# Performance work log

Measured on AMD Instinct MI355X. Metric: run time of the kernel, lower is better.

The kernel has to match this reference:

```python
import jax, jax.numpy as jnp
import numpy as np

B, C, D, J = 8, 2048, 128, 128

def setup_inputs() -> dict:
    key = jax.random.key(0)
    ks = jax.random.split(key, 24)
    s = 0.02
    inp = {
        "operation_features": jax.random.normal(ks[0], (B, C, D), jnp.float32),
        "relations": jax.random.randint(ks[1], (B, C - 2, 2), 0, C, jnp.int64),
        "begins_idx": jax.random.randint(ks[2], (B, J), 0, C, jnp.int64),
        "ends_idx": jax.random.randint(ks[3], (B, J), 0, C, jnp.int64),
        "same_type_mask": (jax.random.uniform(ks[4], (B, C, C)) > 0.5).astype(jnp.float32),
        # BeginEndEncoder
        "W_begin": jax.random.normal(ks[5], (D, D), jnp.float32) * s,
        "b_begin": jnp.zeros((D,), jnp.float32),
        "W_end": jax.random.normal(ks[6], (D, D), jnp.float32) * s,
        "b_end": jnp.zeros((D,), jnp.float32),
        # OperationTimeRelationEncoder.mix: Linear(3D -> D)
        "W_mix3": jax.random.normal(ks[7], (3 * D, D), jnp.float32) * s,
        "b_mix3": jnp.zeros((D,), jnp.float32),
        # SelfAttention (hidden_dim = D)
        "W_qkv": jax.random.normal(ks[8], (D, 3 * D), jnp.float32) * s,
        "b_qkv": jnp.zeros((3 * D,), jnp.float32),
        "w_score": jax.random.normal(ks[9], (2 * D,), jnp.float32) * s,
        "b_score": jnp.zeros((), jnp.float32),
        "W_out": jax.random.normal(ks[10], (D, D), jnp.float32) * s,
        "b_out": jnp.zeros((D,), jnp.float32),
        # block mix: Linear(2D -> D)
        "W_mix2": jax.random.normal(ks[11], (2 * D, D), jnp.float32) * s,
        "b_mix2": jnp.zeros((D,), jnp.float32),
    }
    return inp

def _gather_ops(ops, idx):
    # ops: [B,C,D], idx: [B,M] -> [B,M,D]  (torch.gather along dim 1 with expanded index)
    Bb, _, Dd = ops.shape
    M = idx.shape[1]
    return jnp.take_along_axis(ops, jnp.broadcast_to(idx[:, :, None], (Bb, M, Dd)), axis=1)

def reference(operation_features, relations, begins_idx, ends_idx, same_type_mask,
              W_begin, b_begin, W_end, b_end, W_mix3, b_mix3,
              W_qkv, b_qkv, w_score, b_score, W_out, b_out, W_mix2, b_mix2):
    ops = operation_features
    Dd = ops.shape[-1]
    # --- OperationTimeRelationEncoder ---
    pred = _gather_ops(ops, relations[..., 0])      # [B,C-2,D]
    succ = _gather_ops(ops, relations[..., 1])      # [B,C-2,D]
    concated = jnp.concatenate([ops[:, :-2, :], pred, succ], axis=-1)  # [B,C-2,3D]
    mixed = concated @ W_mix3 + b_mix3              # [B,C-2,D]
    begin_f = _gather_ops(ops, begins_idx) @ W_begin + b_begin  # [B,J,D]
    end_f = _gather_ops(ops, ends_idx) @ W_end + b_end
    begin = jnp.mean(begin_f, axis=1)               # [B,D]
    end = jnp.mean(end_f, axis=1)
    seq = jnp.concatenate([mixed, begin[:, None, :], end[:, None, :]], axis=1)  # [B,C,D]
    # --- SelfAttention (GAT-style additive score, decomposed to avoid CxCx2h blowup) ---
    qkv = ops @ W_qkv + b_qkv                       # [B,C,3D]
    q, k, v = jnp.split(qkv, 3, axis=-1)
    sq = q @ w_score[:Dd]                           # [B,C]  q_i . w_q
    sk = k @ w_score[Dd:]                           # [B,C]  k_j . w_k
    scores = jax.nn.leaky_relu(sq[:, :, None] + sk[:, None, :] + b_score)  # [B,C,C]
    attn = jax.nn.softmax(scores * same_type_mask, axis=-1)                # multiplicative mask, as in torch
    weighted = jnp.einsum('bij,bjd->bid', attn, v)  # [B,C,D]
    same_type = weighted @ W_out + b_out            # [B,C,D]
    # --- final mix ---
    return jnp.concatenate([seq, same_type], axis=-1) @ W_mix2 + b_mix2  # [B,C,D]
```

## Files before the change

### kernel.cpp

```cpp
#include <hip/hip_runtime.h>
#include <cstddef>

typedef __bf16 bf16;
typedef __bf16 bf16x4 __attribute__((ext_vector_type(4)));
typedef __bf16 bf16x8 __attribute__((ext_vector_type(8)));
typedef float  f32x4  __attribute__((ext_vector_type(4)));

#define MFMA16(a, b, c) __builtin_amdgcn_mfma_f32_16x16x32_bf16((a), (b), (c), 0, 0, 0)

#define BB 8
#define CC 2048
#define DD 128
#define JJN 128

#define WS_PK    ((size_t)0)
#define WS_OATT  ((size_t)4194304)
#define WS_OPS16 ((size_t)8388608)
#define WS_SQF   ((size_t)12582912)
#define WS_SKF   ((size_t)12648448)
#define WS_G1T   ((size_t)12713984)
#define WS_G2T   ((size_t)12746752)
#define WS_G3T   ((size_t)12779520)
#define WS_WCT   ((size_t)12812288)
#define WS_GBT   ((size_t)12845056)
#define WS_GET   ((size_t)12877824)
#define WS_UQK   ((size_t)12910592)
#define WS_BBM   ((size_t)12911104)
#define WS_BBB   ((size_t)12911616)
#define WS_BBE   ((size_t)12912128)
#define WS_SC    ((size_t)12912640)

__global__ __launch_bounds__(256) void k_prepcast(
    const float* __restrict__ ops, bf16* __restrict__ ops16,
    const float* __restrict__ Wmix3, const float* __restrict__ Wmix2,
    const float* __restrict__ Wout,  const float* __restrict__ Wbegin,
    const float* __restrict__ Wend,  const float* __restrict__ Wqkv,
    const float* __restrict__ bqkv,  const float* __restrict__ wscore,
    const float* __restrict__ bscore,const float* __restrict__ bmix3,
    const float* __restrict__ bout,  const float* __restrict__ bmix2,
    const float* __restrict__ bbegin,const float* __restrict__ bend,
    bf16* __restrict__ G1T, bf16* __restrict__ G2T, bf16* __restrict__ G3T,
    bf16* __restrict__ WCT, bf16* __restrict__ GBT, bf16* __restrict__ GET,
    bf16* __restrict__ uqk, float* __restrict__ BBM, float* __restrict__ BBB,
    float* __restrict__ BBE, float* __restrict__ sc)
{
    __shared__ bf16  LshT[128 * 132];
    __shared__ float Rsh[128 * 8];
    int wg = blockIdx.x;
    int t  = threadIdx.x;

    if (wg < 1024) {
        size_t i = (size_t)wg * 256 + t;
        f32x4 a = *(const f32x4*)(ops + i * 8);
        f32x4 b = *(const f32x4*)(ops + i * 8 + 4);
        bf16x8 o;
        #pragma unroll
        for (int e = 0; e < 4; ++e) { o[e] = (bf16)a[e]; o[4 + e] = (bf16)b[e]; }
        *(bf16x8*)(ops16 + i * 8) = o;
        return;
    }
    if (wg < 1120) {
        int id  = wg - 1024;
        int mat = id >> 4, sub = id & 15;
        const float* L; const float* R; bf16* O;
        switch (mat) {
            case 0: L = Wmix3;           R = Wmix2;           O = G1T; break;
            case 1: L = Wmix3 + 128*128; R = Wmix2;           O = G2T; break;
            case 2: L = Wmix3 + 256*128; R = Wmix2;           O = G3T; break;
            case 3: L = Wout;            R = Wmix2 + 128*128; O = WCT; break;
            case 4: L = Wbegin;          R = Wmix2;           O = GBT; break;
            default:L = Wend;            R = Wmix2;           O = GET; break;
        }
        int e0 = sub * 8;
        #pragma unroll
        for (int pass = 0; pass < 16; ++pass) {
            int idx = pass * 256 + t;
            int d   = idx >> 5;
            int f0  = (idx & 31) * 4;
            f32x4 v = *(const f32x4*)(L + d * 128 + f0);
            #pragma unroll
            for (int jj = 0; jj < 4; ++jj)
                LshT[(f0 + jj) * 132 + d] = (bf16)v[jj];
        }
        #pragma unroll
        for (int pass = 0; pass < 4; ++pass) {
            int idx = pass * 256 + t;
            int f   = idx >> 3;
            int ee  = idx & 7;
            Rsh[f * 8 + ee] = R[f * 128 + e0 + ee];
        }
        __syncthreads();
        int ee = t >> 5;
        int e  = e0 + ee;
        int d0 = (t & 31) * 4;
        float s[4] = {0.f, 0.f, 0.f, 0.f};
        for (int f = 0; f < 128; ++f) {
            bf16x4 lv = *(const bf16x4*)&LshT[f * 132 + d0];
            float rv = Rsh[f * 8 + ee];
            #pragma unroll
            for (int dd = 0; dd < 4; ++dd)
                s[dd] += (float)lv[dd] * rv;
        }
        #pragma unroll
        for (int dd = 0; dd < 4; ++dd)
            O[e * 128 + d0 + dd] = (bf16)s[dd];
        return;
    }
    if (t < 128) {
        int d = t;
        float su = 0.f, sk_ = 0.f;
        for (int e2 = 0; e2 < 128; ++e2) {
            su  += Wqkv[d*384 + e2]       * wscore[e2];
            sk_ += Wqkv[d*384 + 128 + e2] * wscore[128 + e2];
        }
        uqk[d]       = (bf16)su;
        uqk[128 + d] = (bf16)sk_;
        int e = d;
        float bm = 0.f, bon = 0.f, bb_ = 0.f, be_ = 0.f;
        for (int f = 0; f < 128; ++f) {
            float w2a = Wmix2[f*128 + e];
            float w2b = Wmix2[(128+f)*128 + e];
            bm  += bmix3[f]  * w2a;
            bon += bout[f]   * w2b;
            bb_ += bbegin[f] * w2a;
            be_ += bend[f]   * w2a;
        }
        float bm2 = bmix2[e];
        BBM[e] = bm  + bon + bm2;
        BBB[e] = bb_ + bon + bm2;
        BBE[e] = be_ + bon + bm2;
    } else if (t == 128) {
        float cq = 0.f, ck = 0.f;
        for (int e2 = 0; e2 < 128; ++e2) {
            cq += bqkv[e2]       * wscore[e2];
            ck += bqkv[128 + e2] * wscore[128 + e2];
        }
        sc[0] = cq + bscore[0];
        sc[1] = ck;
    }
}

__global__ __launch_bounds__(256) void k_v(
    const bf16* __restrict__ ops16, const float* __restrict__ Wqkv,
    const float* __restrict__ bqkv, const bf16* __restrict__ uqk,
    const float* __restrict__ sc,
    bf16* __restrict__ PK, float* __restrict__ sqf, float* __restrict__ skf)
{
    __shared__ bf16 A[144 * 136];
    int b  = blockIdx.x >> 4;
    int jt = (blockIdx.x & 15) * 128;
    int t  = threadIdx.x;
    #pragma unroll
    for (int pass = 0; pass < 16; ++pass) {
        int idx = pass * 256 + t;
        int d   = idx >> 5;
        int n0  = (idx & 31) * 4;
        f32x4 v = *(const f32x4*)(Wqkv + d*384 + 256 + n0);
        #pragma unroll
        for (int jj = 0; jj < 4; ++jj)
            A[(n0 + jj)*136 + d] = (bf16)v[jj];
    }
    {
        int row = t >> 7, col = t & 127;
        A[(128 + row)*136 + col] = uqk[row*128 + col];
    }
    for (int idx = t; idx < 14*136; idx += 256)
        A[130*136 + idx] = (bf16)0.f;
    __syncthreads();

    int lane = t & 63, w = t >> 6;
    int m = lane & 15, q = lane >> 4;
    f32x4 acc[9][2];
    #pragma unroll
    for (int rb = 0; rb < 9; ++rb)
        #pragma unroll
        for (int cb = 0; cb < 2; ++cb)
            acc[rb][cb] = {0.f, 0.f, 0.f, 0.f};

    const bf16* opsb = ops16 + (size_t)b * CC * DD;
    #pragma unroll
    for (int kc = 0; kc < 4; ++kc) {
        bf16x8 bfr[2];
        #pragma unroll
        for (int cb = 0; cb < 2; ++cb) {
            int j = jt + w*32 + cb*16 + m;
            bfr[cb] = *(const bf16x8*)(opsb + (size_t)j*DD + kc*32 + q*8);
        }
        #pragma unroll
        for (int rb = 0; rb < 9; ++rb) {
            bf16x8 afr = *(const bf16x8*)&A[(rb*16 + m)*136 + kc*32 + q*8];
            acc[rb][0] = MFMA16(afr, bfr[0], acc[rb][0]);
            acc[rb][1] = MFMA16(afr, bfr[1], acc[rb][1]);
        }
    }
    float cqb = sc[0], ckv = sc[1];
    #pragma unroll
    for (int cb = 0; cb < 2; ++cb) {
        int j = jt + w*32 + cb*16 + m;
        if (q == 0) {
            sqf[b*CC + j] = acc[8][cb][0] + cqb;
            skf[b*CC + j] = acc[8][cb][1] + ckv;
        }
    }
    __syncthreads();
    bf16* pack = A;
    #pragma unroll
    for (int cb = 0; cb < 2; ++cb) {
        int qq_base = cb*2 + (m>>3);
        int e       = m & 7;
        #pragma unroll
        for (int rb = 0; rb < 8; ++rb) {
            #pragma unroll
            for (int r = 0; r < 4; ++r) {
                float v = acc[rb][cb][r] + bqkv[256 + rb*16 + q*4 + r];
                pack[w*4096 + rb*512 + qq_base*128 + (q*4+r)*8 + e] = (bf16)v;
            }
        }
    }
    __syncthreads();
    bf16* pkb = PK + (size_t)b * DD * CC + (size_t)jt * 128;
    #pragma unroll
    for (int pass = 0; pass < 8; ++pass) {
        int lidx = pass * 256 + t;
        *(uint4*)(pkb + (size_t)lidx * 8) = *(const uint4*)&pack[lidx * 8];
    }
}

struct MaskLd { f32x4 v[8]; };

__device__ __forceinline__ MaskLd stage_load(const float* __restrict__ mrow0,
                                             int st, int lane)
{
    MaskLd L;
    int rr0 = lane >> 4, cc = (lane & 15) * 4;
    const float* src = mrow0 + st * 64 + cc;
    #pragma unroll
    for (int k = 0; k < 8; ++k)
        L.v[k] = __builtin_nontemporal_load(
            (const f32x4*)(src + ((size_t)(rr0 + k * 4)) * CC));
    return L;
}

__device__ __forceinline__ void stage_write(const MaskLd& L, bf16* mb,
                                            int buf, int lane)
{
    int rr0 = lane >> 4, cc = (lane & 15) * 4;
    bf16* dst = mb + buf * 2816;
    #pragma unroll
    for (int k = 0; k < 8; ++k) {
        bf16x4 o;
        #pragma unroll
        for (int e = 0; e < 4; ++e) o[e] = (bf16)L.v[k][e];
        *(bf16x4*)(dst + (rr0 + k * 4) * 88 + cc) = o;
    }
}

__device__ __forceinline__ void load_vb(const bf16* __restrict__ pkb, int jc,
                                        int q, int m, bf16x8 vb[8])
{
    #pragma unroll
    for (int nb = 0; nb < 8; ++nb)
        vb[nb] = *(const bf16x8*)(pkb + ((size_t)(((jc*8 + nb)*4 + q)*16 + m)) * 8);
}

__device__ __forceinline__ void substep(const bf16* mb, const float* skb,
    int buf, int st, int sub, int tile, int q, int m, float sq,
    const bf16x8 vb[8], float& lsum, f32x4 acc[8])
{
    bf16x8 mk = *(const bf16x8*)(mb + buf * 2816 + (tile*16 + m) * 88
                                 + sub * 32 + q * 8);
    int jo = st * 64 + sub * 32 + q * 8;
    f32x4 s0 = *(const f32x4*)(skb + jo);
    f32x4 s1 = *(const f32x4*)(skb + jo + 4);
    float sks[8] = {s0[0], s0[1], s0[2], s0[3], s1[0], s1[1], s1[2], s1[3]};
    bf16x8 a;
    #pragma unroll
    for (int e = 0; e < 8; ++e) {
        float tv = sq + sks[e];
        float lr = fmaxf(tv, 0.01f * tv);
        float z  = lr * (float)mk[e];
        float p  = __expf(z);
        lsum += p;
        a[e] = (bf16)p;
    }
    #pragma unroll
    for (int nb = 0; nb < 8; ++nb)
        acc[nb] = MFMA16(a, vb[nb], acc[nb]);
}

__global__ __launch_bounds__(256) void k_att(
    const float* __restrict__ mask, const bf16* __restrict__ PK,
    const float* __restrict__ sqf, const float* __restrict__ skf,
    bf16* __restrict__ Oatt)
{
    __shared__ __align__(16) char smem[53248];
    int t    = threadIdx.x;
    int lane = t & 63, w = t >> 6;
    int b    = blockIdx.x & 7;
    int i0   = (blockIdx.x >> 3) << 5;
    int m = lane & 15, q = lane >> 4;

    bf16*  mbuf = (bf16*)(smem + w * 11264);
    float* skb  = (float*)(smem + 45056 + w * 2048);

    {
        const float* src = skf + b*CC + w*512;
        f32x4 v0 = *(const f32x4*)(src + lane*4);
        f32x4 v1 = *(const f32x4*)(src + 256 + lane*4);
        *(f32x4*)(skb + lane*4) = v0;
        *(f32x4*)(skb + 256 + lane*4) = v1;
    }
    float sq0 = sqf[b*CC + i0 + m];
    float sq1 = sqf[b*CC + i0 + 16 + m];
    const float* mrow0 = mask + ((size_t)(b*CC + i0))*CC + w*512;
    const bf16*  pkb   = PK + (size_t)b * DD * CC;
    int jc0 = w * 16;

    f32x4 acc0[8], acc1[8];
    #pragma unroll
    for (int nb = 0; nb < 8; ++nb) {
        acc0[nb] = {0.f, 0.f, 0.f, 0.f};
        acc1[nb] = {0.f, 0.f, 0.f, 0.f};
    }
    float lsum0 = 0.f, lsum1 = 0.f;

    {   MaskLd r0 = stage_load(mrow0, 0, lane);
        stage_write(r0, mbuf, 0, lane); }
    MaskLd r1 = stage_load(mrow0, 1, lane);
    MaskLd r2 = stage_load(mrow0, 2, lane);

    int buf = 0;
    for (int st = 0; st < 8; ++st) {
        #pragma unroll
        for (int sub = 0; sub < 2; ++sub) {
            bf16x8 vb[8];
            load_vb(pkb, jc0 + st*2 + sub, q, m, vb);
            substep(mbuf, skb, buf, st, sub, 0, q, m, sq0, vb, lsum0, acc0);
            substep(mbuf, skb, buf, st, sub, 1, q, m, sq1, vb, lsum1, acc1);
        }
        if (st + 1 < 8) stage_write(r1, mbuf, buf ^ 1, lane);
        r1 = r2;
        if (st + 3 < 8) r2 = stage_load(mrow0, st + 3, lane);
        buf ^= 1;
    }

    __syncthreads();
    float* Osh = (float*)smem;
    float* Lsh = (float*)(smem + 33792);
    #pragma unroll
    for (int tile = 0; tile < 2; ++tile) {
        float ls = tile ? lsum1 : lsum0;
        ls += __shfl_xor(ls, 16, 64);
        ls += __shfl_xor(ls, 32, 64);
        if (q == 0) Lsh[w*16 + m] = ls;
        const f32x4* acc = tile ? acc1 : acc0;
        #pragma unroll
        for (int nb = 0; nb < 8; ++nb)
            #pragma unroll
            for (int r = 0; r < 4; ++r)
                Osh[(w*16 + q*4 + r)*132 + nb*16 + m] = acc[nb][r];
        __syncthreads();

        int r  = t >> 4;
        int c0 = (t & 15) * 8;
        float l = Lsh[r] + Lsh[16 + r] + Lsh[32 + r] + Lsh[48 + r];
        float inv = 1.0f / l;
        bf16x8 o;
        #pragma unroll
        for (int e = 0; e < 8; ++e) {
            float s = Osh[r*132 + c0 + e] + Osh[(16 + r)*132 + c0 + e]
                    + Osh[(32 + r)*132 + c0 + e] + Osh[(48 + r)*132 + c0 + e];
            o[e] = (bf16)(s * inv);
        }
        *(bf16x8*)(Oatt + ((size_t)(b*CC) + i0 + tile*16 + r)*DD + c0) = o;
        if (tile == 0) __syncthreads();
    }
}

__global__ __launch_bounds__(256) void k_epi(
    const bf16* __restrict__ ops16, const int* __restrict__ relations,
    const int* __restrict__ begins, const int* __restrict__ ends,
    const bf16* __restrict__ Oatt,
    const bf16* __restrict__ G1T, const bf16* __restrict__ G2T,
    const bf16* __restrict__ G3T, const bf16* __restrict__ WCT,
    const bf16* __restrict__ GBT, const bf16* __restrict__ GET,
    const float* __restrict__ BBM, const float* __restrict__ BBB,
    const float* __restrict__ BBE, float* __restrict__ out)
{
    __shared__ bf16 Abuf[32 * 136];
    __shared__ bf16 Bbuf[128 * 136];
    int t  = threadIdx.x;

    if (blockIdx.x >= 512) {
        __shared__ float meanv[2][128];
        int eidx  = (blockIdx.x - 512) * 2 + (t >> 7);
        int b     = eidx >> 1, which = eidx & 1;
        int tl    = t & 127;
        const int* idx = which ? (ends + b*JJN) : (begins + b*JJN);
        const bf16* opsb = ops16 + (size_t)b * CC * DD;
        float s = 0.f;
        for (int j = 0; j < JJN; ++j) {
            int rr = idx[j];
            s += (float)opsb[(size_t)rr*DD + tl];
        }
        meanv[t >> 7][tl] = s * (1.0f / (float)JJN);
        __syncthreads();
        const bf16* G   = which ? GET : GBT;
        const float* Bv = which ? BBE : BBB;
        const bf16* orow = Oatt + ((size_t)b*CC + (CC - 2 + which)) * DD;
        float a = Bv[tl];
        const bf16* gr = G + tl*128;
        const bf16* wr = WCT + tl*128;
        const float* mv = meanv[t >> 7];
        for (int d = 0; d < 128; ++d) {
            a += mv[d] * (float)gr[d];
            a += (float)orow[d] * (float)wr[d];
        }
        out[((size_t)b*CC + (CC - 2 + which))*DD + tl] = a;
        return;
    }

    int b  = blockIdx.x >> 6;
    int c0 = (blockIdx.x & 63) * 32;
    int lane = t & 63, w = t >> 6;
    int m = lane & 15, q = lane >> 4;

    f32x4 acc[2][2];
    #pragma unroll
    for (int rb = 0; rb < 2; ++rb)
        #pragma unroll
        for (int cb = 0; cb < 2; ++cb)
            acc[rb][cb] = {0.f, 0.f, 0.f, 0.f};

    const bf16* Bsrc[4] = {G1T, G2T, G3T, WCT};
    int arow = t >> 3, ao = (t & 7) * 16;
    int brow = t >> 1, bo = (t & 1) * 64;
    int c = c0 + arow;

    for (int term = 0; term < 4; ++term) {
        const bf16* src;
        if (term == 0)      src = ops16 + ((size_t)(b*CC + c)) * DD;
        else if (term == 3) src = Oatt  + ((size_t)(b*CC + c)) * DD;
        else {
            int ridx = relations[((size_t)b*(CC-2) + min(c, CC-3))*2 + (term - 1)];
            src = ops16 + ((size_t)(b*CC) + ridx) * DD;
        }
        *(uint4*)&Abuf[arow*136 + ao]     = *(const uint4*)(src + ao);
        *(uint4*)&Abuf[arow*136 + ao + 8] = *(const uint4*)(src + ao + 8);

        const uint4* bs = (const uint4*)(Bsrc[term] + brow*128 + bo);
        uint4* bd = (uint4*)&Bbuf[brow*136 + bo];
        #pragma unroll
        for (int ii = 0; ii < 8; ++ii) bd[ii] = bs[ii];
        __syncthreads();

        #pragma unroll
        for (int kc = 0; kc < 4; ++kc) {
            bf16x8 bfr[2];
            #pragma unroll
            for (int cb = 0; cb < 2; ++cb)
                bfr[cb] = *(const bf16x8*)&Bbuf[(w*32 + cb*16 + m)*136 + kc*32 + q*8];
            #pragma unroll
            for (int rb = 0; rb < 2; ++rb) {
                bf16x8 afr = *(const bf16x8*)&Abuf[(rb*16 + m)*136 + kc*32 + q*8];
                acc[rb][0] = MFMA16(afr, bfr[0], acc[rb][0]);
                acc[rb][1] = MFMA16(afr, bfr[1], acc[rb][1]);
            }
        }
        __syncthreads();
    }
    #pragma unroll
    for (int cb = 0; cb < 2; ++cb) {
        int col = w*32 + cb*16 + m;
        float bias = BBM[col];
        #pragma unroll
        for (int rb = 0; rb < 2; ++rb) {
            #pragma unroll
            for (int r = 0; r < 4; ++r) {
                int cg = c0 + rb*16 + q*4 + r;
                if (cg < CC - 2)
                    out[((size_t)(b*CC) + cg)*DD + col] = acc[rb][cb][r] + bias;
            }
        }
    }
}

extern "C" void kernel_launch(void* const* d_in, const int* in_sizes, int n_in,
                              void* d_out, int out_size, void* d_ws, size_t ws_size,
                              hipStream_t stream)
{
    const float* ops      = (const float*)d_in[0];
    const int*  relations = (const int*)d_in[1];
    const int*  begins    = (const int*)d_in[2];
    const int*  ends      = (const int*)d_in[3];
    const float* mask     = (const float*)d_in[4];
    const float* Wbegin   = (const float*)d_in[5];
    const float* bbegin   = (const float*)d_in[6];
    const float* Wend     = (const float*)d_in[7];
    const float* bend     = (const float*)d_in[8];
    const float* Wmix3    = (const float*)d_in[9];
    const float* bmix3    = (const float*)d_in[10];
    const float* Wqkv     = (const float*)d_in[11];
    const float* bqkv     = (const float*)d_in[12];
    const float* wscore   = (const float*)d_in[13];
    const float* bscore   = (const float*)d_in[14];
    const float* Wout     = (const float*)d_in[15];
    const float* bout     = (const float*)d_in[16];
    const float* Wmix2    = (const float*)d_in[17];
    const float* bmix2    = (const float*)d_in[18];
    float* outp = (float*)d_out;

    char* ws = (char*)d_ws;
    bf16*  PK    = (bf16*)(ws + WS_PK);
    bf16*  Oatt  = (bf16*)(ws + WS_OATT);
    bf16*  OPS16 = (bf16*)(ws + WS_OPS16);
    float* sqf   = (float*)(ws + WS_SQF);
    float* skf   = (float*)(ws + WS_SKF);
    bf16*  G1T   = (bf16*)(ws + WS_G1T);
    bf16*  G2T   = (bf16*)(ws + WS_G2T);
    bf16*  G3T   = (bf16*)(ws + WS_G3T);
    bf16*  WCT   = (bf16*)(ws + WS_WCT);
    bf16*  GBT   = (bf16*)(ws + WS_GBT);
    bf16*  GET   = (bf16*)(ws + WS_GET);
    bf16*  UQK   = (bf16*)(ws + WS_UQK);
    float* BBM   = (float*)(ws + WS_BBM);
    float* BBB   = (float*)(ws + WS_BBB);
    float* BBE   = (float*)(ws + WS_BBE);
    float* SC    = (float*)(ws + WS_SC);

    k_prepcast<<<dim3(1121), dim3(256), 0, stream>>>(
        ops, OPS16,
        Wmix3, Wmix2, Wout, Wbegin, Wend, Wqkv, bqkv, wscore, bscore,
        bmix3, bout, bmix2, bbegin, bend,
        G1T, G2T, G3T, WCT, GBT, GET, UQK, BBM, BBB, BBE, SC);

    k_v<<<dim3(128), dim3(256), 0, stream>>>(
        OPS16, Wqkv, bqkv, UQK, SC, PK, sqf, skf);

    k_att<<<dim3(512), dim3(256), 0, stream>>>(
        mask, PK, sqf, skf, Oatt);

    k_epi<<<dim3(520), dim3(256), 0, stream>>>(
        OPS16, relations, begins, ends, Oatt,
        G1T, G2T, G3T, WCT, GBT, GET, BBM, BBB, BBE, outp);
}
```

Measured before the change: 295.1 us.

## Reorder prep blocks to start long tail work first and coalesce tail matvecs

The serial bias/score-vector prep block moves to block 0 so it is scheduled first rather than trailing the cast blocks. Its loads are staged through shared memory with vector reads, and the final scalar reduction is split across threads. The same reordering puts the begin/end tail blocks of the epilogue first, and they now read transposed (row-major by d) weight copies so global accesses coalesce. This adds extra transposed weight buffers and strided stores in the prep kernel.

```diff
diff --git a/kernel.cpp b/kernel.cpp
--- a/kernel.cpp
+++ b/kernel.cpp
@@ -29,6 +29,9 @@
 #define WS_BBB   ((size_t)12911616)
 #define WS_BBE   ((size_t)12912128)
 #define WS_SC    ((size_t)12912640)
+#define WS_WCN   ((size_t)12913152)
+#define WS_GBN   ((size_t)12945920)
+#define WS_GEN   ((size_t)12978688)
 
 __global__ __launch_bounds__(256) void k_prepcast(
     const float* __restrict__ ops, bf16* __restrict__ ops16,
@@ -41,6 +44,7 @@
     const float* __restrict__ bbegin,const float* __restrict__ bend,
     bf16* __restrict__ G1T, bf16* __restrict__ G2T, bf16* __restrict__ G3T,
     bf16* __restrict__ WCT, bf16* __restrict__ GBT, bf16* __restrict__ GET,
+    bf16* __restrict__ WCN, bf16* __restrict__ GBN, bf16* __restrict__ GEN,
     bf16* __restrict__ uqk, float* __restrict__ BBM, float* __restrict__ BBB,
     float* __restrict__ BBE, float* __restrict__ sc)
 {
@@ -49,27 +53,111 @@
     int wg = blockIdx.x;
     int t  = threadIdx.x;
 
-    if (wg < 1024) {
-        size_t i = (size_t)wg * 256 + t;
-        f32x4 a = *(const f32x4*)(ops + i * 8);
-        f32x4 b = *(const f32x4*)(ops + i * 8 + 4);
-        bf16x8 o;
-        #pragma unroll
-        for (int e = 0; e < 4; ++e) { o[e] = (bf16)a[e]; o[4 + e] = (bf16)b[e]; }
-        *(bf16x8*)(ops16 + i * 8) = o;
+    if (wg == 0) {
+        for (int half = 0; half < 2; ++half) {
+            #pragma unroll
+            for (int pass = 0; pass < 16; ++pass) {
+                int idx = pass * 256 + t;
+                int d   = idx >> 5;
+                int e0  = (idx & 31) * 4;
+                f32x4 v = *(const f32x4*)(Wqkv + d*384 + half*128 + e0);
+                #pragma unroll
+                for (int jj = 0; jj < 4; ++jj)
+                    LshT[(e0 + jj)*132 + d] = (bf16)v[jj];
+            }
+            if (t < 32) {
+                f32x4 wv = *(const f32x4*)(wscore + half*128 + t*4);
+                #pragma unroll
+                for (int jj = 0; jj < 4; ++jj) Rsh[t*4 + jj] = wv[jj];
+            }
+            __syncthreads();
+            if (t < 128) {
+                float s = 0.f;
+                for (int e = 0; e < 128; ++e)
+                    s += (float)LshT[e*132 + t] * Rsh[e];
+                uqk[half*128 + t] = (bf16)s;
+            }
+            __syncthreads();
+        }
+        float bm = 0.f, bb_ = 0.f, be_ = 0.f, bon = 0.f;
+        for (int half = 0; half < 2; ++half) {
+            #pragma unroll
+            for (int pass = 0; pass < 16; ++pass) {
+                int idx = pass * 256 + t;
+                int f   = idx >> 5;
+                int e0  = (idx & 31) * 4;
+                f32x4 v = *(const f32x4*)(Wmix2 + (size_t)(half*128 + f)*128 + e0);
+                #pragma unroll
+                for (int jj = 0; jj < 4; ++jj)
+                    LshT[f*132 + e0 + jj] = (bf16)v[jj];
+            }
+            if (t < 32) {
+                if (half == 0) {
+                    f32x4 v0 = *(const f32x4*)(bmix3  + t*4);
+                    f32x4 v1 = *(const f32x4*)(bbegin + t*4);
+                    f32x4 v2 = *(const f32x4*)(bend   + t*4);
+                    #pragma unroll
+                    for (int jj = 0; jj < 4; ++jj) {
+                        Rsh[t*4 + jj]       = v0[jj];
+                        Rsh[128 + t*4 + jj] = v1[jj];
+                        Rsh[256 + t*4 + jj] = v2[jj];
+                    }
+                } else {
+                    f32x4 v3 = *(const f32x4*)(bout + t*4);
+                    #pragma unroll
+                    for (int jj = 0; jj < 4; ++jj) Rsh[t*4 + jj] = v3[jj];
+                }
+            }
+            __syncthreads();
+            if (t < 128) {
+                if (half == 0) {
+                    for (int f = 0; f < 128; ++f) {
+                        float wv = (float)LshT[f*132 + t];
+                        bm  += Rsh[f]       * wv;
+                        bb_ += Rsh[128 + f] * wv;
+                        be_ += Rsh[256 + f] * wv;
+                    }
+                } else {
+                    for (int f = 0; f < 128; ++f)
+                        bon += Rsh[f] * (float)LshT[f*132 + t];
+                }
+            }
+            __syncthreads();
+        }
+        if (t < 128) {
+            float bm2 = bmix2[t];
+            BBM[t] = bm  + bon + bm2;
+            BBB[t] = bb_ + bon + bm2;
+            BBE[t] = be_ + bon + bm2;
+        }
+        if (t >= 128) {
+            int e2 = t - 128;
+            Rsh[512 + e2] = bqkv[e2]       * wscore[e2];
+            Rsh[640 + e2] = bqkv[128 + e2] * wscore[128 + e2];
+        }
+        __syncthreads();
+        if (t == 0) {
+            float cq = 0.f, ck = 0.f;
+            for (int e2 = 0; e2 < 128; ++e2) {
+                cq += Rsh[512 + e2];
+                ck += Rsh[640 + e2];
+            }
+            sc[0] = cq + bscore[0];
+            sc[1] = ck;
+        }
         return;
     }
-    if (wg < 1120) {
-        int id  = wg - 1024;
+    if (wg <= 96) {
+        int id  = wg - 1;
         int mat = id >> 4, sub = id & 15;
-        const float* L; const float* R; bf16* O;
+        const float* L; const float* R; bf16* O; bf16* O2;
         switch (mat) {
-            case 0: L = Wmix3;           R = Wmix2;           O = G1T; break;
-            case 1: L = Wmix3 + 128*128; R = Wmix2;           O = G2T; break;
-            case 2: L = Wmix3 + 256*128; R = Wmix2;           O = G3T; break;
-            case 3: L = Wout;            R = Wmix2 + 128*128; O = WCT; break;
-            case 4: L = Wbegin;          R = Wmix2;           O = GBT; break;
-            default:L = Wend;            R = Wmix2;           O = GET; break;
+            case 0: L = Wmix3;           R = Wmix2;           O = G1T; O2 = nullptr; break;
+            case 1: L = Wmix3 + 128*128; R = Wmix2;           O = G2T; O2 = nullptr; break;
+            case 2: L = Wmix3 + 256*128; R = Wmix2;           O = G3T; O2 = nullptr; break;
+            case 3: L = Wout;            R = Wmix2 + 128*128; O = WCT; O2 = WCN; break;
+            case 4: L = Wbegin;          R = Wmix2;           O = GBT; O2 = GBN; break;
+            default:L = Wend;            R = Wmix2;           O = GET; O2 = GEN; break;
         }
         int e0 = sub * 8;
         #pragma unroll
@@ -102,42 +190,19 @@
                 s[dd] += (float)lv[dd] * rv;
         }
         #pragma unroll
-        for (int dd = 0; dd < 4; ++dd)
+        for (int dd = 0; dd < 4; ++dd) {
             O[e * 128 + d0 + dd] = (bf16)s[dd];
+            if (O2) O2[(d0 + dd) * 128 + e] = (bf16)s[dd];
+        }
         return;
     }
-    if (t < 128) {
-        int d = t;
-        float su = 0.f, sk_ = 0.f;
-        for (int e2 = 0; e2 < 128; ++e2) {
-            su  += Wqkv[d*384 + e2]       * wscore[e2];
-            sk_ += Wqkv[d*384 + 128 + e2] * wscore[128 + e2];
-        }
-        uqk[d]       = (bf16)su;
-        uqk[128 + d] = (bf16)sk_;
-        int e = d;
-        float bm = 0.f, bon = 0.f, bb_ = 0.f, be_ = 0.f;
-        for (int f = 0; f < 128; ++f) {
-            float w2a = Wmix2[f*128 + e];
-            float w2b = Wmix2[(128+f)*128 + e];
-            bm  += bmix3[f]  * w2a;
-            bon += bout[f]   * w2b;
-            bb_ += bbegin[f] * w2a;
-            be_ += bend[f]   * w2a;
-        }
-        float bm2 = bmix2[e];
-        BBM[e] = bm  + bon + bm2;
-        BBB[e] = bb_ + bon + bm2;
-        BBE[e] = be_ + bon + bm2;
-    } else if (t == 128) {
-        float cq = 0.f, ck = 0.f;
-        for (int e2 = 0; e2 < 128; ++e2) {
-            cq += bqkv[e2]       * wscore[e2];
-            ck += bqkv[128 + e2] * wscore[128 + e2];
-        }
-        sc[0] = cq + bscore[0];
-        sc[1] = ck;
-    }
+    size_t i = (size_t)(wg - 97) * 256 + t;
+    f32x4 a = *(const f32x4*)(ops + i * 8);
+    f32x4 b = *(const f32x4*)(ops + i * 8 + 4);
+    bf16x8 o;
+    #pragma unroll
+    for (int e = 0; e < 4; ++e) { o[e] = (bf16)a[e]; o[4 + e] = (bf16)b[e]; }
+    *(bf16x8*)(ops16 + i * 8) = o;
 }
 
 __global__ __launch_bounds__(256) void k_v(
@@ -383,7 +448,8 @@
     const bf16* __restrict__ Oatt,
     const bf16* __restrict__ G1T, const bf16* __restrict__ G2T,
     const bf16* __restrict__ G3T, const bf16* __restrict__ WCT,
-    const bf16* __restrict__ GBT, const bf16* __restrict__ GET,
+    const bf16* __restrict__ GBN, const bf16* __restrict__ GEN,
+    const bf16* __restrict__ WCN,
     const float* __restrict__ BBM, const float* __restrict__ BBB,
     const float* __restrict__ BBE, float* __restrict__ out)
 {
@@ -391,37 +457,37 @@
     __shared__ bf16 Bbuf[128 * 136];
     int t  = threadIdx.x;
 
-    if (blockIdx.x >= 512) {
+    if (blockIdx.x < 8) {
         __shared__ float meanv[2][128];
-        int eidx  = (blockIdx.x - 512) * 2 + (t >> 7);
+        int eidx  = blockIdx.x * 2 + (t >> 7);
         int b     = eidx >> 1, which = eidx & 1;
         int tl    = t & 127;
         const int* idx = which ? (ends + b*JJN) : (begins + b*JJN);
         const bf16* opsb = ops16 + (size_t)b * CC * DD;
-        float s = 0.f;
-        for (int j = 0; j < JJN; ++j) {
-            int rr = idx[j];
-            s += (float)opsb[(size_t)rr*DD + tl];
-        }
-        meanv[t >> 7][tl] = s * (1.0f / (float)JJN);
+        float s0 = 0.f, s1 = 0.f;
+        for (int j = 0; j < JJN; j += 2) {
+            int r0 = idx[j], r1 = idx[j+1];
+            s0 += (float)opsb[(size_t)r0*DD + tl];
+            s1 += (float)opsb[(size_t)r1*DD + tl];
+        }
+        meanv[t >> 7][tl] = (s0 + s1) * (1.0f / (float)JJN);
         __syncthreads();
-        const bf16* G   = which ? GET : GBT;
+        const bf16* G   = which ? GEN : GBN;
         const float* Bv = which ? BBE : BBB;
         const bf16* orow = Oatt + ((size_t)b*CC + (CC - 2 + which)) * DD;
         float a = Bv[tl];
-        const bf16* gr = G + tl*128;
-        const bf16* wr = WCT + tl*128;
         const float* mv = meanv[t >> 7];
         for (int d = 0; d < 128; ++d) {
-            a += mv[d] * (float)gr[d];
-            a += (float)orow[d] * (float)wr[d];
+            a += mv[d] * (float)G[d*128 + tl];
+            a += (float)orow[d] * (float)WCN[d*128 + tl];
         }
         out[((size_t)b*CC + (CC - 2 + which))*DD + tl] = a;
         return;
     }
 
-    int b  = blockIdx.x >> 6;
-    int c0 = (blockIdx.x & 63) * 32;
+    int gid = blockIdx.x - 8;
+    int b  = gid >> 6;
+    int c0 = (gid & 63) * 32;
     int lane = t & 63, w = t >> 6;
     int m = lane & 15, q = lane >> 4;
 
@@ -522,6 +588,9 @@
     bf16*  WCT   = (bf16*)(ws + WS_WCT);
     bf16*  GBT   = (bf16*)(ws + WS_GBT);
     bf16*  GET   = (bf16*)(ws + WS_GET);
+    bf16*  WCN   = (bf16*)(ws + WS_WCN);
+    bf16*  GBN   = (bf16*)(ws + WS_GBN);
+    bf16*  GEN   = (bf16*)(ws + WS_GEN);
     bf16*  UQK   = (bf16*)(ws + WS_UQK);
     float* BBM   = (float*)(ws + WS_BBM);
     float* BBB   = (float*)(ws + WS_BBB);
@@ -532,7 +601,8 @@
         ops, OPS16,
         Wmix3, Wmix2, Wout, Wbegin, Wend, Wqkv, bqkv, wscore, bscore,
         bmix3, bout, bmix2, bbegin, bend,
-        G1T, G2T, G3T, WCT, GBT, GET, UQK, BBM, BBB, BBE, SC);
+        G1T, G2T, G3T, WCT, GBT, GET, WCN, GBN, GEN,
+        UQK, BBM, BBB, BBE, SC);
 
     k_v<<<dim3(128), dim3(256), 0, stream>>>(
         OPS16, Wqkv, bqkv, UQK, SC, PK, sqf, skf);
@@ -542,5 +612,5 @@
 
     k_epi<<<dim3(520), dim3(256), 0, stream>>>(
         OPS16, relations, begins, ends, Oatt,
-        G1T, G2T, G3T, WCT, GBT, GET, BBM, BBB, BBE, outp);
-}
+        G1T, G2T, G3T, WCT, GBN, GEN, WCN, BBM, BBB, BBE, outp);
+}
```

Measured after the change: 287.2 us. 2.7% less time.
